# Kernel optimization log

Measured on AMD Instinct MI355X. Metric: run time of the kernel, lower is better.

The kernel has to match this reference:

```python
import jax, jax.numpy as jnp
import numpy as np

N, E = 100000, 1600000
N_IN, NHID, HEADS, NOUT = 64, 16, 4, 64
NEG_SLOPE = 0.2


def _p(key, shape, scale=0.1):
    return jax.random.normal(key, shape, dtype=jnp.float32) * scale


def setup_inputs() -> dict:
    key = jax.random.key(0)
    ks = jax.random.split(key, 16)
    H, C1 = HEADS, NHID
    inp = {
        "x": jax.random.normal(ks[0], (N, N_IN), dtype=jnp.float32),
        "edge_index": jax.random.randint(ks[1], (2, E), 0, N, dtype=jnp.int64),
        "frame_mask": jnp.ones((N,), dtype=bool),
        # layer 1: GATv2Conv(N_IN -> NHID, heads=H, concat=True)
        "Wl1": _p(ks[2], (N_IN, H * C1)),
        "bl1": jnp.zeros((H * C1,), jnp.float32),
        "Wr1": _p(ks[3], (N_IN, H * C1)),
        "br1": jnp.zeros((H * C1,), jnp.float32),
        "att1": _p(ks[4], (H, C1)),
        "bo1": jnp.zeros((H * C1,), jnp.float32),
        # layer 2: GATv2Conv(H*NHID -> NOUT, heads=H, concat=False)
        "Wl2": _p(ks[5], (H * C1, H * NOUT)),
        "bl2": jnp.zeros((H * NOUT,), jnp.float32),
        "Wr2": _p(ks[6], (H * C1, H * NOUT)),
        "br2": jnp.zeros((H * NOUT,), jnp.float32),
        "att2": _p(ks[7], (H, NOUT)),
        "bo2": jnp.zeros((NOUT,), jnp.float32),
    }
    return inp


def gatv2_layer(x, src, dst, Wl, bl, Wr, br, att, bo, concat):
    n = x.shape[0]
    H, C = att.shape
    xl = (x @ Wl + bl).reshape(n, H, C)  # source-side transform
    xr = (x @ Wr + br).reshape(n, H, C)  # target-side transform
    # per-edge GATv2 attention: att . leaky_relu(xl[j] + xr[i])
    e = jax.nn.leaky_relu(xl[src] + xr[dst], NEG_SLOPE)  # [E', H, C]
    score = jnp.einsum('ehc,hc->eh', e, att)             # [E', H]
    # scatter-softmax over edges grouped by destination node
    m = jax.ops.segment_max(score, dst, num_segments=n)
    ex = jnp.exp(score - m[dst])
    denom = jax.ops.segment_sum(ex, dst, num_segments=n)
    alpha = ex / (denom[dst] + 1e-16)                    # [E', H]
    out = jax.ops.segment_sum(alpha[:, :, None] * xl[src], dst, num_segments=n)
    out = out.reshape(n, H * C) if concat else out.mean(axis=1)
    return out + bo


def reference(x, edge_index, frame_mask, Wl1, bl1, Wr1, br1, att1, bo1,
              Wl2, bl2, Wr2, br2, att2, bo2):
    n = x.shape[0]
    loops = jnp.arange(n, dtype=edge_index.dtype)
    src = jnp.concatenate([edge_index[0], loops])  # add self-loops (PyG default)
    dst = jnp.concatenate([edge_index[1], loops])
    h = gatv2_layer(x, src, dst, Wl1, bl1, Wr1, br1, att1, bo1, concat=True)
    h = jax.nn.relu(h)
    h = gatv2_layer(h, src, dst, Wl2, bl2, Wr2, br2, att2, bo2, concat=False)
    return jax.nn.relu(h)
```

## Files before the change

kernel.cpp:

```cpp
#include <hip/hip_runtime.h>
#include <hip/hip_bf16.h>
#include <cstdint>
#include <cstddef>

#define NNODES 100000
#define NEDGES 1600000
#define EPLUS  (NEDGES + NNODES)
#define NHEADS 4
#define NB     ((NNODES + 255) / 256)

typedef __hip_bfloat16 bf16;
typedef unsigned short u16;
typedef __attribute__((ext_vector_type(8))) short bf16x8;
typedef __attribute__((ext_vector_type(4))) float f32x4;

#define F_X    0
#define F_WL1  1
#define F_BL1  2
#define F_WR1  3
#define F_BR1  4
#define F_ATT1 5
#define F_BO1  6
#define F_WL2  7
#define F_BL2  8
#define F_WR2  9
#define F_BR2  10
#define F_ATT2 11
#define F_BO2  12
#define F_EI64 13

__device__ __forceinline__ float u2f(u16 s) { return __uint_as_float(((unsigned)s) << 16); }
__device__ __forceinline__ u16  f2u(float f) {
    return __bfloat16_as_ushort(__float2bfloat16(f));
}
__device__ __forceinline__ float ld_any(const void* p, long i, int f32) {
    return f32 ? ((const float*)p)[i] : u2f(((const u16*)p)[i]);
}

__global__ void detect_all(const u16* x, const u16* Wl1, const u16* bl1,
                           const u16* Wr1, const u16* br1, const u16* att1,
                           const u16* bo1, const u16* Wl2, const u16* bl2,
                           const u16* Wr2, const u16* br2, const u16* att2,
                           const u16* bo2, const int* ei, int* flags) {
    const int t = threadIdx.x;
    const u16* ptrs[13] = {x, Wl1, bl1, Wr1, br1, att1, bo1,
                           Wl2, bl2, Wr2, br2, att2, bo2};
    const int cnts[13] = {NNODES * 64, 64 * 64, 64, 64 * 64, 64, 64, 64,
                          64 * 256, 256, 64 * 256, 256, 256, 64};
    if (t < 13) {
        const u16* p = ptrs[t];
        const int cnt = cnts[t];
        int weird = 0, n = 0;
        for (int k = 0; k < 128; ++k) {
            int idx = 2 * k;
            if (idx >= cnt) break;
            u16 v = p[idx];
            n++;
            int ex = (v >> 7) & 0xFF;
            if (v != 0 && (ex < 96 || ex > 143)) weird++;
        }
        flags[t] = (weird * 4 > n) ? 1 : 0;
    } else if (t == 13) {
        int any = 0;
        for (int k = 0; k < 64; ++k) any |= ei[2 * k + 1];
        flags[F_EI64] = (any == 0) ? 1 : 0;
    }
}

__device__ __forceinline__ void edge_sd(const int* __restrict__ ei, int i64,
                                        int e, int& s, int& d) {
    if (e >= NEDGES) { s = d = e - NEDGES; return; }
    if (i64) {
        const long long* p = (const long long*)ei;
        s = (int)p[e]; d = (int)p[NEDGES + e];
    } else {
        s = ei[e]; d = ei[NEDGES + e];
    }
    s = min(max(s, 0), NNODES - 1);
    d = min(max(d, 0), NNODES - 1);
}

#define XB 6250
#define WB 160
#define BB 3
#define HB 6250
__global__ __launch_bounds__(256)
void conv_all(const void* __restrict__ x,
              const void* __restrict__ Wl1, const void* __restrict__ Wr1,
              const void* __restrict__ Wl2, const void* __restrict__ Wr2,
              const void* __restrict__ bl1, const void* __restrict__ br1,
              const void* __restrict__ bl2, const void* __restrict__ br2,
              const int* __restrict__ ei, const int* __restrict__ flags,
              u16* __restrict__ xc, u16* __restrict__ wt1l, u16* __restrict__ wt1r,
              u16* __restrict__ wt2l, u16* __restrict__ wt2r,
              u16* __restrict__ bcs, int* __restrict__ cnt) {
    int b = blockIdx.x;
    if (b < XB) {
        const long i4 = ((long)b * 256 + threadIdx.x) * 4;
        if (i4 < (long)NNODES * 64) {
            if (flags[F_X]) {
                const float4 v = *(const float4*)((const float*)x + i4);
                ushort4 o; o.x=f2u(v.x); o.y=f2u(v.y); o.z=f2u(v.z); o.w=f2u(v.w);
                *(ushort4*)(xc + i4) = o;
            } else {
                *(ushort4*)(xc + i4) = *(const ushort4*)((const u16*)x + i4);
            }
        }
        return;
    }
    b -= XB;
    if (b < WB) {
        const int e = b * 256 + threadIdx.x;
        const void* W; u16* wt; int M, fwi, local;
        if (e < 4096)        { W = Wl1; wt = wt1l; M = 64;  fwi = F_WL1; local = e; }
        else if (e < 8192)   { W = Wr1; wt = wt1r; M = 64;  fwi = F_WR1; local = e - 4096; }
        else if (e < 24576)  { W = Wl2; wt = wt2l; M = 256; fwi = F_WL2; local = e - 8192; }
        else                 { W = Wr2; wt = wt2r; M = 256; fwi = F_WR2; local = e - 24576; }
        const int m = local >> 6, k = local & 63;
        wt[local] = f2u(ld_any(W, (long)k * M + m, flags[fwi]));
        return;
    }
    b -= WB;
    if (b < BB) {
        const int t = b * 256 + threadIdx.x;
        if (t < 64)       bcs[t] = f2u(ld_any(bl1, t,       flags[F_BL1]));
        else if (t < 128) bcs[t] = f2u(ld_any(br1, t - 64,  flags[F_BR1]));
        else if (t < 384) bcs[t] = f2u(ld_any(bl2, t - 128, flags[F_BL2]));
        else if (t < 640) bcs[t] = f2u(ld_any(br2, t - 384, flags[F_BR2]));
        return;
    }
    b -= BB;
    {
        const int e = b * 256 + threadIdx.x;
        if (e >= NEDGES) return;
        int d;
        if (flags[F_EI64]) d = (int)((const long long*)ei)[NEDGES + e];
        else               d = ei[NEDGES + e];
        d = min(max(d, 0), NNODES - 1);
        atomicAdd(&cnt[d], 1);
    }
}

__global__ __launch_bounds__(256)
void scan1_kernel(const int* __restrict__ cnt, int* __restrict__ tmp,
                  int* __restrict__ bsum) {
    __shared__ int sh[256];
    const int idx = blockIdx.x * 256 + threadIdx.x;
    int v = (idx < NNODES) ? cnt[idx] + 1 : 0;
    sh[threadIdx.x] = v;
    __syncthreads();
    for (int off = 1; off < 256; off <<= 1) {
        int t = (threadIdx.x >= off) ? sh[threadIdx.x - off] : 0;
        __syncthreads();
        sh[threadIdx.x] += t;
        __syncthreads();
    }
    if (idx < NNODES) tmp[idx] = sh[threadIdx.x];
    if (threadIdx.x == 255) bsum[blockIdx.x] = sh[255];
}

__global__ __launch_bounds__(512)
void scan2_kernel(int* __restrict__ bsum) {
    __shared__ int sh[512];
    const int t = threadIdx.x;
    sh[t] = (t < NB) ? bsum[t] : 0;
    __syncthreads();
    for (int off = 1; off < 512; off <<= 1) {
        int v = (t >= off) ? sh[t - off] : 0;
        __syncthreads();
        sh[t] += v;
        __syncthreads();
    }
    if (t < NB) bsum[t] = sh[t];
}

__global__ __launch_bounds__(256)
void scan3_kernel(const int* __restrict__ tmp, const int* __restrict__ bsum,
                  int* __restrict__ row_ptr) {
    const int idx = blockIdx.x * 256 + threadIdx.x;
    if (idx < NNODES) {
        int off = (blockIdx.x > 0) ? bsum[blockIdx.x - 1] : 0;
        row_ptr[idx + 1] = tmp[idx] + off;
    }
    if (idx == 0) row_ptr[0] = 0;
}

__global__ __launch_bounds__(256)
void fill_kernel(const int* __restrict__ ei, const int* __restrict__ flags,
                 const int* __restrict__ row_ptr, int* __restrict__ cur,
                 int* __restrict__ csr_src) {
    const int e = blockIdx.x * 256 + threadIdx.x;
    if (e >= EPLUS) return;
    int s, d;
    edge_sd(ei, flags[F_EI64], e, s, d);
    int slot = row_ptr[d] + atomicAdd(&cur[d], 1);
    csr_src[slot] = s;
}

template<int M, int RPB>
__global__ __launch_bounds__(256)
void gemm_mfma(const u16* __restrict__ xc,
               const u16* __restrict__ wtl, const u16* __restrict__ wtr,
               const u16* __restrict__ bcl, const u16* __restrict__ bcr,
               u16* __restrict__ outl, u16* __restrict__ outr) {
    constexpr int MT = RPB / 16;
    constexpr int NT = M / 64;
    const u16* wt = blockIdx.y ? wtr : wtl;
    const u16* bc = blockIdx.y ? bcr : bcl;
    u16* out      = blockIdx.y ? outr : outl;
    const int wave = threadIdx.x >> 6;
    const int lane = threadIdx.x & 63;
    const int quad = lane >> 4;
    const int l16  = lane & 15;
    const int row0 = blockIdx.x * RPB;
    const int col0 = wave * (M / 4);

    bf16x8 bfrag[NT][2];
#pragma unroll
    for (int nt = 0; nt < NT; ++nt)
#pragma unroll
        for (int c = 0; c < 2; ++c)
            bfrag[nt][c] = *(const bf16x8*)(wt +
                ((size_t)(col0 + nt * 16 + l16) * 64 + c * 32 + quad * 8));

    f32x4 acc[MT][NT];
#pragma unroll
    for (int mt = 0; mt < MT; ++mt)
#pragma unroll
        for (int nt = 0; nt < NT; ++nt)
            acc[mt][nt] = f32x4{0.f, 0.f, 0.f, 0.f};

#pragma unroll
    for (int mt = 0; mt < MT; ++mt) {
        int row = row0 + mt * 16 + l16;
        row = (row < NNODES) ? row : (NNODES - 1);
#pragma unroll
        for (int c = 0; c < 2; ++c) {
            bf16x8 afrag = *(const bf16x8*)(xc + ((size_t)row * 64 + c * 32 + quad * 8));
#pragma unroll
            for (int nt = 0; nt < NT; ++nt)
                acc[mt][nt] = __builtin_amdgcn_mfma_f32_16x16x32_bf16(
                    afrag, bfrag[nt][c], acc[mt][nt], 0, 0, 0);
        }
    }

#pragma unroll
    for (int mt = 0; mt < MT; ++mt) {
#pragma unroll
        for (int nt = 0; nt < NT; ++nt) {
            const int col = col0 + nt * 16 + l16;
            const float bias = u2f(bc[col]);
#pragma unroll
            for (int r = 0; r < 4; ++r) {
                const int row = row0 + mt * 16 + quad * 4 + r;
                if (row < NNODES)
                    out[(size_t)row * M + col] = f2u(acc[mt][nt][r] + bias);
            }
        }
    }
}

__global__ __launch_bounds__(256)
void gat_l1(const u16* __restrict__ xl, const u16* __restrict__ xr,
            const int* __restrict__ row_ptr, const int* __restrict__ csr_src,
            const void* __restrict__ att, const void* __restrict__ bo,
            const int* __restrict__ flags, u16* __restrict__ out) {
    const int d = blockIdx.x * 4 + (threadIdx.x >> 6);
    if (d >= NNODES) return;
    const int lane = threadIdx.x & 63;
    const int q = lane >> 4;
    const int l = lane & 15;
    const int fatt = flags[F_ATT1];

    float attv[4], rv[4];
#pragma unroll
    for (int j = 0; j < 4; ++j)
        attv[j] = ld_any(att, l * 4 + j, fatt);
    {
        ushort4 r = *(const ushort4*)(xr + (size_t)d * 64 + l * 4);
        rv[0]=u2f(r.x); rv[1]=u2f(r.y); rv[2]=u2f(r.z); rv[3]=u2f(r.w);
    }

    const int beg = row_ptr[d], end = row_ptr[d + 1];
    float denom = 1e-16f;
    float acc[4] = {0.f, 0.f, 0.f, 0.f};

    ushort4 a4;
    {
        int e0 = beg + q;
        int idx = (e0 < end) ? e0 : (end - 1);
        a4 = *(const ushort4*)(xl + (size_t)csr_src[idx] * 64 + l * 4);
    }

    for (int base = beg; base < end; base += 4) {
        float lv[4];
        lv[0]=u2f(a4.x); lv[1]=u2f(a4.y); lv[2]=u2f(a4.z); lv[3]=u2f(a4.w);
        if (base + 4 < end) {
            int en = base + 4 + q;
            int idx = (en < end) ? en : (end - 1);
            a4 = *(const ushort4*)(xl + (size_t)csr_src[idx] * 64 + l * 4);
        }
        float part = 0.f;
#pragma unroll
        for (int j = 0; j < 4; ++j) {
            float v = lv[j] + rv[j];
            v = fmaxf(v, 0.2f * v);
            part = fmaf(v, attv[j], part);
        }
        part += __shfl_xor(part, 1, 64);
        part += __shfl_xor(part, 2, 64);
        float ex = __expf(fminf(part, 60.f));
        ex = (base + q < end) ? ex : 0.f;
        denom += ex;
#pragma unroll
        for (int j = 0; j < 4; ++j)
            acc[j] = fmaf(ex, lv[j], acc[j]);
    }

    denom += __shfl_xor(denom, 16, 64);
    denom += __shfl_xor(denom, 32, 64);
#pragma unroll
    for (int j = 0; j < 4; ++j) {
        acc[j] += __shfl_xor(acc[j], 16, 64);
        acc[j] += __shfl_xor(acc[j], 32, 64);
    }
    const float inv = 1.f / denom;

    if (lane < 16) {
        const int fbo = flags[F_BO1];
        ushort4 o;
        u16* op = (u16*)&o;
#pragma unroll
        for (int j = 0; j < 4; ++j) {
            float v = acc[j] * inv + ld_any(bo, l * 4 + j, fbo);
            op[j] = f2u((v > 0.f) ? v : 0.f);
        }
        *(ushort4*)(out + (size_t)d * 64 + l * 4) = o;
    }
}

__global__ __launch_bounds__(256)
void gat_l2(const u16* __restrict__ xl, const u16* __restrict__ xr,
            const int* __restrict__ row_ptr, const int* __restrict__ csr_src,
            const void* __restrict__ att, const void* __restrict__ bo,
            const int* __restrict__ flags, float* __restrict__ out) {
    const int d = blockIdx.x * 4 + (threadIdx.x >> 6);
    if (d >= NNODES) return;
    const int lane = threadIdx.x & 63;
    const int fatt = flags[F_ATT2];

    float attv[4], rv[4];
#pragma unroll
    for (int j = 0; j < 4; ++j)
        attv[j] = ld_any(att, lane * 4 + j, fatt);
    {
        ushort4 r = *(const ushort4*)(xr + (size_t)d * 256 + lane * 4);
        rv[0]=u2f(r.x); rv[1]=u2f(r.y); rv[2]=u2f(r.z); rv[3]=u2f(r.w);
    }

    const int beg = row_ptr[d], end = row_ptr[d + 1];
    float denom = 1e-16f;
    float acc[4] = {0.f, 0.f, 0.f, 0.f};

    ushort4 b0, b1;
    b0 = *(const ushort4*)(xl + (size_t)csr_src[beg] * 256 + lane * 4);
    if (beg + 1 < end)
        b1 = *(const ushort4*)(xl + (size_t)csr_src[beg + 1] * 256 + lane * 4);

    for (int i = beg; i < end; i += 2) {
        {
            float lv[4];
            lv[0]=u2f(b0.x); lv[1]=u2f(b0.y); lv[2]=u2f(b0.z); lv[3]=u2f(b0.w);
            if (i + 2 < end)
                b0 = *(const ushort4*)(xl + (size_t)csr_src[i + 2] * 256 + lane * 4);
            float part = 0.f;
#pragma unroll
            for (int j = 0; j < 4; ++j) {
                float v = lv[j] + rv[j];
                v = fmaxf(v, 0.2f * v);
                part = fmaf(v, attv[j], part);
            }
#pragma unroll
            for (int off = 8; off >= 1; off >>= 1)
                part += __shfl_xor(part, off, 64);
            float ex = __expf(fminf(part, 60.f));
            denom += ex;
#pragma unroll
            for (int j = 0; j < 4; ++j)
                acc[j] = fmaf(ex, lv[j], acc[j]);
        }
        if (i + 1 < end) {
            float lv[4];
            lv[0]=u2f(b1.x); lv[1]=u2f(b1.y); lv[2]=u2f(b1.z); lv[3]=u2f(b1.w);
            if (i + 3 < end)
                b1 = *(const ushort4*)(xl + (size_t)csr_src[i + 3] * 256 + lane * 4);
            float part = 0.f;
#pragma unroll
            for (int j = 0; j < 4; ++j) {
                float v = lv[j] + rv[j];
                v = fmaxf(v, 0.2f * v);
                part = fmaf(v, attv[j], part);
            }
#pragma unroll
            for (int off = 8; off >= 1; off >>= 1)
                part += __shfl_xor(part, off, 64);
            float ex = __expf(fminf(part, 60.f));
            denom += ex;
#pragma unroll
            for (int j = 0; j < 4; ++j)
                acc[j] = fmaf(ex, lv[j], acc[j]);
        }
    }

    const float inv = 1.f / denom;
#pragma unroll
    for (int j = 0; j < 4; ++j) {
        acc[j] *= inv;
        acc[j] += __shfl_xor(acc[j], 16, 64);
        acc[j] += __shfl_xor(acc[j], 32, 64);
    }
    if (lane < 16) {
        const int fbo = flags[F_BO2];
        float4 o;
        float* op = (float*)&o;
#pragma unroll
        for (int j = 0; j < 4; ++j) {
            float v = acc[j] * 0.25f + ld_any(bo, lane * 4 + j, fbo);
            op[j] = (v > 0.f) ? v : 0.f;
        }
        *(float4*)(out + (size_t)d * 64 + lane * 4) = o;
    }
}

__global__ void plant_kernel(float* out, float code) {
    if (code > 0.f) out[0] = code;
}

extern "C" void kernel_launch(void* const* d_in, const int* in_sizes, int n_in,
                              void* d_out, int out_size, void* d_ws, size_t ws_size,
                              hipStream_t stream) {
    int ix = -1, iei = -1;
    int i4096[2], i16384[2], i64s[5], i256[3];
    int c4 = 0, c16 = 0, c64 = 0, c256 = 0;
    bool extra = false;
    for (int i = 0; i < n_in; ++i) {
        int sz = in_sizes[i];
        if (sz == 6400000)      { if (ix < 0) ix = i; else extra = true; }
        else if (sz == 3200000) { if (iei < 0) iei = i; else extra = true; }
        else if (sz == 4096)    { if (c4  < 2) i4096[c4]  = i; c4++;  }
        else if (sz == 16384)   { if (c16 < 2) i16384[c16] = i; c16++; }
        else if (sz == 64)      { if (c64 < 5) i64s[c64]  = i; c64++; }
        else if (sz == 256)     { if (c256 < 3) i256[c256] = i; c256++; }
        else if (sz == 100000 || sz == 1) {  }
        else extra = true;
    }
    bool ok = (ix >= 0) && (iei >= 0) && (c4 == 2) && (c16 == 2)
              && (c64 == 5) && (c256 == 3) && !extra;
    float code = 0.f;
    if (!ok) {
        code = 50000.f + 100.f * (float)n_in;
        ix = 0; iei = 1;
        i4096[0] = 3;  i4096[1] = 5;
        i64s[0] = 4; i64s[1] = 6; i64s[2] = 7; i64s[3] = 8; i64s[4] = 14;
        i16384[0] = 9; i16384[1] = 11;
        i256[0] = 10; i256[1] = 12; i256[2] = 13;
    }

    const u16* x    = (const u16*)d_in[ix];
    const int* ei   = (const int*)d_in[iei];
    const u16* Wl1  = (const u16*)d_in[i4096[0]];
    const u16* Wr1  = (const u16*)d_in[i4096[1]];
    const u16* bl1  = (const u16*)d_in[i64s[0]];
    const u16* br1  = (const u16*)d_in[i64s[1]];
    const u16* att1 = (const u16*)d_in[i64s[2]];
    const u16* bo1  = (const u16*)d_in[i64s[3]];
    const u16* bo2  = (const u16*)d_in[i64s[4]];
    const u16* Wl2  = (const u16*)d_in[i16384[0]];
    const u16* Wr2  = (const u16*)d_in[i16384[1]];
    const u16* bl2  = (const u16*)d_in[i256[0]];
    const u16* br2  = (const u16*)d_in[i256[1]];
    const u16* att2 = (const u16*)d_in[i256[2]];

    char* ws = (char*)d_ws;
    u16* xlb     = (u16*)(ws);
    u16* xrb     = (u16*)(ws + 51200000);
    u16* hbuf    = (u16*)(ws + 102400000);
    u16* xc      = (u16*)(ws + 115200000);
    int* row_ptr = (int*)(ws + 128000000);
    int* cnt     = (int*)(ws + 128400016);
    int* tmp     = (int*)(ws + 128800016);
    int* bsum    = (int*)(ws + 129200016);
    int* csr_src = (int*)(ws + 129201600);
    u16* wt1l    = (u16*)(ws + 136001600);
    u16* wt1r    = (u16*)(ws + 136009792);
    u16* wt2l    = (u16*)(ws + 136017984);
    u16* wt2r    = (u16*)(ws + 136050752);
    u16* bcs     = (u16*)(ws + 136083520);
    int* flags   = (int*)(ws + 136084800);
    const size_t need = 136084864;
    if (ws_size < need) {
        float c2 = 60000.f + (float)(ws_size >> 20);
        code = (c2 > code) ? c2 : code;
    }

    const int node_grid = (NNODES + 3) / 4;
    const int ep_grid   = (EPLUS + 255) / 256;

    detect_all<<<1, 64, 0, stream>>>(x, Wl1, bl1, Wr1, br1, att1, bo1,
                                     Wl2, bl2, Wr2, br2, att2, bo2, ei, flags);

    (void)hipMemsetAsync(cnt, 0, (size_t)NNODES * 4, stream);
    conv_all<<<XB + WB + BB + HB, 256, 0, stream>>>(
        x, Wl1, Wr1, Wl2, Wr2, bl1, br1, bl2, br2, ei, flags,
        xc, wt1l, wt1r, wt2l, wt2r, bcs, cnt);

    scan1_kernel<<<NB, 256, 0, stream>>>(cnt, tmp, bsum);
    scan2_kernel<<<1, 512, 0, stream>>>(bsum);
    scan3_kernel<<<NB, 256, 0, stream>>>(tmp, bsum, row_ptr);
    (void)hipMemsetAsync(cnt, 0, (size_t)NNODES * 4, stream);
    fill_kernel<<<ep_grid, 256, 0, stream>>>(ei, flags, row_ptr, cnt, csr_src);

    gemm_mfma<64, 128><<<dim3((NNODES + 127) / 128, 2), 256, 0, stream>>>(
        xc, wt1l, wt1r, bcs, bcs + 64, xlb, xrb);
    gat_l1<<<node_grid, 256, 0, stream>>>(
        xlb, xrb, row_ptr, csr_src, att1, bo1, flags, hbuf);

    gemm_mfma<256, 64><<<dim3((NNODES + 63) / 64, 2), 256, 0, stream>>>(
        hbuf, wt2l, wt2r, bcs + 128, bcs + 384, xlb, xrb);
    gat_l2<<<node_grid, 256, 0, stream>>>(
        xlb, xrb, row_ptr, csr_src, att2, bo2, flags, (float*)d_out);

    plant_kernel<<<1, 1, 0, stream>>>((float*)d_out, code);
}
```

Baseline: 667.9 us.

## Split layer-2 wavefront into two half-waves processing two edges concurrently

The layer-2 aggregation kernel now assigns each half of a 64-lane wavefront to a different edge. Each lane loads 8 bf16 features with 16-byte loads and uses packed float2 math. This halves the serial edge-loop trip count and the per-edge cross-lane reductions, and raises the number of outstanding gather loads. The cost is an extra cross-half reduction at the end and masked wasted work when the edge count is odd.

```diff
diff --git a/kernel.cpp b/kernel.cpp
--- a/kernel.cpp
+++ b/kernel.cpp
@@ -13,6 +13,7 @@
 typedef unsigned short u16;
 typedef __attribute__((ext_vector_type(8))) short bf16x8;
 typedef __attribute__((ext_vector_type(4))) float f32x4;
+typedef __attribute__((ext_vector_type(2))) float v2f;
 
 #define F_X    0
 #define F_WL1  1
@@ -35,6 +36,12 @@
 }
 __device__ __forceinline__ float ld_any(const void* p, long i, int f32) {
     return f32 ? ((const float*)p)[i] : u2f(((const u16*)p)[i]);
+}
+__device__ __forceinline__ v2f cvt2(unsigned p) {
+    v2f r;
+    r.x = __uint_as_float(p << 16);
+    r.y = __uint_as_float(p & 0xffff0000u);
+    return r;
 }
 
 __global__ void detect_all(const u16* x, const u16* Wl1, const u16* bl1,
@@ -347,88 +354,94 @@
     const int d = blockIdx.x * 4 + (threadIdx.x >> 6);
     if (d >= NNODES) return;
     const int lane = threadIdx.x & 63;
+    const int half = lane >> 5;
+    const int l    = lane & 31;
     const int fatt = flags[F_ATT2];
 
-    float attv[4], rv[4];
-#pragma unroll
-    for (int j = 0; j < 4; ++j)
-        attv[j] = ld_any(att, lane * 4 + j, fatt);
+    v2f attv[4], rv[4];
+#pragma unroll
+    for (int j = 0; j < 4; ++j) {
+        v2f a;
+        a.x = ld_any(att, l * 8 + 2 * j,     fatt);
+        a.y = ld_any(att, l * 8 + 2 * j + 1, fatt);
+        attv[j] = a;
+    }
     {
-        ushort4 r = *(const ushort4*)(xr + (size_t)d * 256 + lane * 4);
-        rv[0]=u2f(r.x); rv[1]=u2f(r.y); rv[2]=u2f(r.z); rv[3]=u2f(r.w);
+        uint4 r = *(const uint4*)(xr + (size_t)d * 256 + l * 8);
+        rv[0] = cvt2(r.x); rv[1] = cvt2(r.y); rv[2] = cvt2(r.z); rv[3] = cvt2(r.w);
     }
 
     const int beg = row_ptr[d], end = row_ptr[d + 1];
     float denom = 1e-16f;
-    float acc[4] = {0.f, 0.f, 0.f, 0.f};
-
-    ushort4 b0, b1;
-    b0 = *(const ushort4*)(xl + (size_t)csr_src[beg] * 256 + lane * 4);
-    if (beg + 1 < end)
-        b1 = *(const ushort4*)(xl + (size_t)csr_src[beg + 1] * 256 + lane * 4);
-
-    for (int i = beg; i < end; i += 2) {
-        {
-            float lv[4];
-            lv[0]=u2f(b0.x); lv[1]=u2f(b0.y); lv[2]=u2f(b0.z); lv[3]=u2f(b0.w);
-            if (i + 2 < end)
-                b0 = *(const ushort4*)(xl + (size_t)csr_src[i + 2] * 256 + lane * 4);
-            float part = 0.f;
-#pragma unroll
-            for (int j = 0; j < 4; ++j) {
-                float v = lv[j] + rv[j];
-                v = fmaxf(v, 0.2f * v);
-                part = fmaf(v, attv[j], part);
-            }
-#pragma unroll
-            for (int off = 8; off >= 1; off >>= 1)
-                part += __shfl_xor(part, off, 64);
-            float ex = __expf(fminf(part, 60.f));
-            denom += ex;
-#pragma unroll
-            for (int j = 0; j < 4; ++j)
-                acc[j] = fmaf(ex, lv[j], acc[j]);
-        }
-        if (i + 1 < end) {
-            float lv[4];
-            lv[0]=u2f(b1.x); lv[1]=u2f(b1.y); lv[2]=u2f(b1.z); lv[3]=u2f(b1.w);
-            if (i + 3 < end)
-                b1 = *(const ushort4*)(xl + (size_t)csr_src[i + 3] * 256 + lane * 4);
-            float part = 0.f;
-#pragma unroll
-            for (int j = 0; j < 4; ++j) {
-                float v = lv[j] + rv[j];
-                v = fmaxf(v, 0.2f * v);
-                part = fmaf(v, attv[j], part);
-            }
-#pragma unroll
-            for (int off = 8; off >= 1; off >>= 1)
-                part += __shfl_xor(part, off, 64);
-            float ex = __expf(fminf(part, 60.f));
-            denom += ex;
-#pragma unroll
-            for (int j = 0; j < 4; ++j)
-                acc[j] = fmaf(ex, lv[j], acc[j]);
-        }
-    }
-
+    v2f acc[4];
+#pragma unroll
+    for (int j = 0; j < 4; ++j) acc[j] = (v2f){0.f, 0.f};
+
+    uint4 raw;
+    {
+        int idx = beg + half;
+        idx = (idx < end) ? idx : (end - 1);
+        raw = *(const uint4*)(xl + (size_t)csr_src[idx] * 256 + l * 8);
+    }
+
+    for (int base = beg; base < end; base += 2) {
+        v2f lv[4];
+        lv[0] = cvt2(raw.x); lv[1] = cvt2(raw.y);
+        lv[2] = cvt2(raw.z); lv[3] = cvt2(raw.w);
+        if (base + 2 < end) {
+            int idx = base + 2 + half;
+            idx = (idx < end) ? idx : (end - 1);
+            raw = *(const uint4*)(xl + (size_t)csr_src[idx] * 256 + l * 8);
+        }
+        v2f p = (v2f){0.f, 0.f};
+#pragma unroll
+        for (int j = 0; j < 4; ++j) {
+            v2f v = lv[j] + rv[j];
+            v2f t = v * 0.2f;
+            v.x = fmaxf(v.x, t.x);
+            v.y = fmaxf(v.y, t.y);
+            p += v * attv[j];
+        }
+        float part = p.x + p.y;
+        part += __shfl_xor(part, 1, 64);
+        part += __shfl_xor(part, 2, 64);
+        part += __shfl_xor(part, 4, 64);
+        float ex = __expf(fminf(part, 60.f));
+        ex = (base + half < end) ? ex : 0.f;
+        denom += ex;
+#pragma unroll
+        for (int j = 0; j < 4; ++j)
+            acc[j] += lv[j] * ex;
+    }
+
+    denom += __shfl_xor(denom, 32, 64);
+#pragma unroll
+    for (int j = 0; j < 4; ++j) {
+        acc[j].x += __shfl_xor(acc[j].x, 32, 64);
+        acc[j].y += __shfl_xor(acc[j].y, 32, 64);
+    }
     const float inv = 1.f / denom;
 #pragma unroll
     for (int j = 0; j < 4; ++j) {
         acc[j] *= inv;
-        acc[j] += __shfl_xor(acc[j], 16, 64);
-        acc[j] += __shfl_xor(acc[j], 32, 64);
-    }
-    if (lane < 16) {
+        acc[j].x += __shfl_xor(acc[j].x, 8, 64);
+        acc[j].y += __shfl_xor(acc[j].y, 8, 64);
+        acc[j].x += __shfl_xor(acc[j].x, 16, 64);
+        acc[j].y += __shfl_xor(acc[j].y, 16, 64);
+    }
+    if (lane < 8) {
         const int fbo = flags[F_BO2];
-        float4 o;
-        float* op = (float*)&o;
-#pragma unroll
-        for (int j = 0; j < 4; ++j) {
-            float v = acc[j] * 0.25f + ld_any(bo, lane * 4 + j, fbo);
-            op[j] = (v > 0.f) ? v : 0.f;
-        }
-        *(float4*)(out + (size_t)d * 64 + lane * 4) = o;
+        float vv[8];
+#pragma unroll
+        for (int j = 0; j < 4; ++j) { vv[2*j] = acc[j].x; vv[2*j+1] = acc[j].y; }
+#pragma unroll
+        for (int k = 0; k < 8; ++k) {
+            float v = vv[k] * 0.25f + ld_any(bo, l * 8 + k, fbo);
+            vv[k] = (v > 0.f) ? v : 0.f;
+        }
+        float* po = out + (size_t)d * 64 + l * 8;
+        *(float4*)po       = make_float4(vv[0], vv[1], vv[2], vv[3]);
+        *(float4*)(po + 4) = make_float4(vv[4], vv[5], vv[6], vv[7]);
     }
 }
 
```

Result: no change. 659.6 us (-1.2%).
